# Performance work log

Hardware: AMD Instinct MI355X
Metric: run time of the kernel (lower is better)

The kernel has to match this reference:

```python
import jax, jax.numpy as jnp
import numpy as np

D_MODEL = 2048
N_HEADS = 16
KV_HEADS = 4
HEAD_DIM = D_MODEL // N_HEADS  # 128
B, T = 2, 2048


def setup_inputs() -> dict:
    key = jax.random.key(0)
    ks = jax.random.split(key, 8)
    s = 1.0 / np.sqrt(D_MODEL)
    x = jax.random.normal(ks[0], (B, T, D_MODEL), dtype=jnp.float32)
    # Linear weights stored as (in_features, out_features); y = x @ W
    Wq = jax.random.normal(ks[1], (D_MODEL, D_MODEL), dtype=jnp.float32) * s
    Wk = jax.random.normal(ks[2], (D_MODEL, KV_HEADS * HEAD_DIM), dtype=jnp.float32) * s
    Wv = jax.random.normal(ks[3], (D_MODEL, KV_HEADS * HEAD_DIM), dtype=jnp.float32) * s
    Wo = jax.random.normal(ks[4], (D_MODEL, D_MODEL), dtype=jnp.float32) * s
    weight_logits = jnp.ones((KV_HEADS,), dtype=jnp.float32)
    weight_values = jnp.ones((KV_HEADS,), dtype=jnp.float32)
    # additive causal mask (1, 1, T, T): 0 on/below diag, -inf above
    neg_inf = jnp.float32(-1e30)
    causal = jnp.tril(jnp.ones((T, T), dtype=bool))
    attn_mask = jnp.where(causal, jnp.float32(0.0), neg_inf)[None, None]
    return {"x": x, "attn_mask": attn_mask, "Wq": Wq, "Wk": Wk, "Wv": Wv,
            "Wo": Wo, "weight_logits": weight_logits, "weight_values": weight_values}


def reference(x, attn_mask, Wq, Wk, Wv, Wo, weight_logits, weight_values):
    Bx, Tx, _ = x.shape
    H, G, D = N_HEADS, KV_HEADS, HEAD_DIM
    group_size = H // G
    head_to_group = jnp.arange(H) // group_size  # (H,)

    q = (x @ Wq).reshape(Bx, Tx, H, D).transpose(0, 2, 1, 3)  # (B,H,T,D)
    k = (x @ Wk).reshape(Bx, Tx, G, D).transpose(0, 2, 1, 3)  # (B,G,T,D)
    v = (x @ Wv).reshape(Bx, Tx, G, D).transpose(0, 2, 1, 3)  # (B,G,T,D)

    # GQA expansion: gather kv groups per head
    k_g = k[:, head_to_group]  # (B,H,T,D)
    v_g = v[:, head_to_group]  # (B,H,T,D)
    # (use_value_weight=False: weight_values unused)

    logit_scale = weight_logits[head_to_group][None, :, None, None]  # (1,H,1,1)
    inv_sqrt_d = jnp.float32(1.0 / np.sqrt(D))
    logits = jnp.einsum('bhqd,bhkd->bhqk', q, k_g) * inv_sqrt_d * logit_scale
    logits = logits + attn_mask
    attn = jax.nn.softmax(logits, axis=-1)  # dropout p=0 -> identity
    y = jnp.einsum('bhqk,bhkd->bhqd', attn, v_g)
    y = y.transpose(0, 2, 1, 3).reshape(Bx, Tx, H * D)
    return y @ Wo
```

## Files before the change

### kernel.cpp

```cpp
#include <hip/hip_runtime.h>
#include <hip/hip_bf16.h>

#define TT 2048
#define DM 2048
#define NH 16
#define KVH 4
#define HD 128

typedef __attribute__((ext_vector_type(8))) short bs8;
typedef __attribute__((ext_vector_type(4))) float fx4;
typedef __attribute__((ext_vector_type(4))) unsigned short us4;
typedef __attribute__((ext_vector_type(8))) unsigned short us8;

#if __has_builtin(__builtin_amdgcn_exp2f)
#define EXP2(x) __builtin_amdgcn_exp2f(x)
#else
#define EXP2(x) exp2f(x)
#endif

__device__ inline unsigned short f2b(float f) {
  __hip_bfloat16 h = __float2bfloat16(f);
  return *reinterpret_cast<unsigned short*>(&h);
}

__device__ inline float b2f(unsigned short u) {
  unsigned int v = ((unsigned int)u) << 16;
  return *reinterpret_cast<float*>(&v);
}

__device__ inline void gld_lds16(const ushort* g, ushort* l) {
  __builtin_amdgcn_global_load_lds(
      (const __attribute__((address_space(1))) void*)g,
      (__attribute__((address_space(3))) void*)l,
      16, 0, 0);
}

__global__ __launch_bounds__(256) void prep_kernel(
    const float* __restrict__ x, const float* __restrict__ Wq,
    const float* __restrict__ Wk, const float* __restrict__ Wv,
    const float* __restrict__ Wo, ushort* __restrict__ xb,
    ushort* __restrict__ Wqkvt, ushort* __restrict__ Wot) {
  int tx = threadIdx.x, ty = threadIdx.y;
  if (blockIdx.z == 2) {
    int lin = (blockIdx.y * 96 + blockIdx.x) * 256 + ty * 32 + tx;
#pragma unroll
    for (int it = 0; it < 2; ++it) {
      int i = lin + it * (6144 * 256);
      if (i < (TT * 2 * DM) / 4) {
        float4 v = ((const float4*)x)[i];
        us4 o = {f2b(v.x), f2b(v.y), f2b(v.z), f2b(v.w)};
        ((us4*)xb)[i] = o;
      }
    }
    return;
  }
  __shared__ float t[32][33];
  int n0 = blockIdx.x * 32, k0 = blockIdx.y * 32;
  if (blockIdx.z == 0) {
    const float* src;
    int srcN, col0;
    if (n0 < 2048) { src = Wq; srcN = 2048; col0 = n0; }
    else if (n0 < 2560) { src = Wk; srcN = 512; col0 = n0 - 2048; }
    else { src = Wv; srcN = 512; col0 = n0 - 2560; }
    for (int jj = 0; jj < 4; ++jj)
      t[ty + jj * 8][tx] = src[(size_t)(k0 + ty + jj * 8) * srcN + col0 + tx];
    __syncthreads();
    for (int jj = 0; jj < 4; ++jj)
      Wqkvt[(size_t)(n0 + ty + jj * 8) * 2048 + k0 + tx] = f2b(t[tx][ty + jj * 8]);
  } else {
    if (n0 >= 2048) return;
    for (int jj = 0; jj < 4; ++jj)
      t[ty + jj * 8][tx] = Wo[(size_t)(k0 + ty + jj * 8) * 2048 + n0 + tx];
    __syncthreads();
    for (int jj = 0; jj < 4; ++jj)
      Wot[(size_t)(n0 + ty + jj * 8) * 2048 + k0 + tx] = f2b(t[tx][ty + jj * 8]);
  }
}

#define EPI_STRIDE 136
__global__ __launch_bounds__(256) void gemm_qkv(const ushort* __restrict__ A,
                                                const ushort* __restrict__ Bt,
                                                ushort* __restrict__ qo,
                                                ushort* __restrict__ ko,
                                                ushort* __restrict__ vo,
                                                int K) {
  __shared__ alignas(16) ushort smem[128 * EPI_STRIDE];
  ushort* As = smem;
  ushort* Bs = smem + 8192;
  const int tid = threadIdx.x;
  const int lane = tid & 63;
  const int wid = tid >> 6;
  const int wm = wid >> 1, wn = wid & 1;
  const int quad = lane >> 4, l16 = lane & 15;
  const int bm = blockIdx.y * 128, bn = blockIdx.x * 128;

  fx4 acc[4][4];
  for (int i = 0; i < 4; ++i)
    for (int j = 0; j < 4; ++j) acc[i][j] = (fx4){0.f, 0.f, 0.f, 0.f};

  const int r8 = lane >> 3, s8 = lane & 7;
  for (int k0 = 0; k0 < K; k0 += 64) {
    for (int i = 0; i < 4; ++i) {
      int m = i * 32 + wid * 8 + r8;
      int c = s8 ^ (m & 7);
      gld_lds16(A + (size_t)(bm + m) * K + k0 + c * 8, As + (i * 32 + wid * 8) * 64);
      gld_lds16(Bt + (size_t)(bn + m) * K + k0 + c * 8, Bs + (i * 32 + wid * 8) * 64);
    }
    __syncthreads();
    for (int ks = 0; ks < 2; ++ks) {
      bs8 af[4], bf[4];
      for (int mt = 0; mt < 4; ++mt) {
        int m = wm * 64 + mt * 16 + l16;
        int c = ks * 4 + quad;
        int slot = c ^ (m & 7);
        af[mt] = *(const bs8*)(As + m * 64 + slot * 8);
      }
      for (int nt = 0; nt < 4; ++nt) {
        int n = wn * 64 + nt * 16 + l16;
        int c = ks * 4 + quad;
        int slot = c ^ (n & 7);
        bf[nt] = *(const bs8*)(Bs + n * 64 + slot * 8);
      }
      for (int mt = 0; mt < 4; ++mt)
        for (int nt = 0; nt < 4; ++nt)
          acc[mt][nt] = __builtin_amdgcn_mfma_f32_16x16x32_bf16(af[mt], bf[nt],
                                                                acc[mt][nt], 0, 0, 0);
    }
    __syncthreads();
  }

  for (int mt = 0; mt < 4; ++mt)
    for (int nt = 0; nt < 4; ++nt)
      for (int r = 0; r < 4; ++r) {
        int row = wm * 64 + mt * 16 + quad * 4 + r;
        int col = wn * 64 + nt * 16 + l16;
        smem[row * EPI_STRIDE + col] = f2b(acc[mt][nt][r]);
      }
  __syncthreads();
  if (bn < 2560) {
    const int rsel = tid >> 4;
    const int csel = tid & 15;
    for (int ii = 0; ii < 8; ++ii) {
      int row = ii * 16 + rsel;
      us8 chunk = *(const us8*)(smem + row * EPI_STRIDE + csel * 8);
      int row_g = bm + row;
      int colc = bn + csel * 8;
      if (bn < 2048) {
        *(us8*)(qo + (size_t)row_g * 2048 + colc) = chunk;
      } else {
        int b = row_g >> 11, t = row_g & 2047;
        int kc = colc - 2048;
        int gg = kc >> 7, d = kc & 127;
        *(us8*)(ko + ((size_t)(b * KVH + gg) * TT + t) * HD + d) = chunk;
      }
    }
  } else {
    const int gg = (bn - 2560) >> 7;
    const int b = bm >> 11;
    const int t0 = bm & 2047;
    const int tc = tid & 15;
    const int drow = tid >> 4;
    for (int it = 0; it < 8; ++it) {
      int d = it * 16 + drow;
      us8 pw;
#pragma unroll
      for (int j = 0; j < 8; ++j) {
        int jj = (j + tc) & 7;
        pw[jj] = smem[(tc * 8 + jj) * EPI_STRIDE + d];
      }
      *(us8*)(vo + ((size_t)(b * KVH + gg) * HD + d) * TT + t0 + tc * 8) = pw;
    }
  }
}

__global__ __launch_bounds__(256) void gemm_out(const ushort* __restrict__ A,
                                                const ushort* __restrict__ Bt,
                                                float* __restrict__ Cout,
                                                int N, int K) {
  __shared__ alignas(16) ushort smem[128 * EPI_STRIDE];
  ushort* As = smem;
  ushort* Bs = smem + 8192;
  const int tid = threadIdx.x;
  const int lane = tid & 63;
  const int wid = tid >> 6;
  const int wm = wid >> 1, wn = wid & 1;
  const int quad = lane >> 4, l16 = lane & 15;
  const int bm = blockIdx.y * 128, bn = blockIdx.x * 128;

  fx4 acc[4][4];
  for (int i = 0; i < 4; ++i)
    for (int j = 0; j < 4; ++j) acc[i][j] = (fx4){0.f, 0.f, 0.f, 0.f};

  const int r8 = lane >> 3, s8 = lane & 7;
  for (int k0 = 0; k0 < K; k0 += 64) {
    for (int i = 0; i < 4; ++i) {
      int m = i * 32 + wid * 8 + r8;
      int c = s8 ^ (m & 7);
      gld_lds16(A + (size_t)(bm + m) * K + k0 + c * 8, As + (i * 32 + wid * 8) * 64);
      gld_lds16(Bt + (size_t)(bn + m) * K + k0 + c * 8, Bs + (i * 32 + wid * 8) * 64);
    }
    __syncthreads();
    for (int ks = 0; ks < 2; ++ks) {
      bs8 af[4], bf[4];
      for (int mt = 0; mt < 4; ++mt) {
        int m = wm * 64 + mt * 16 + l16;
        int c = ks * 4 + quad;
        int slot = c ^ (m & 7);
        af[mt] = *(const bs8*)(As + m * 64 + slot * 8);
      }
      for (int nt = 0; nt < 4; ++nt) {
        int n = wn * 64 + nt * 16 + l16;
        int c = ks * 4 + quad;
        int slot = c ^ (n & 7);
        bf[nt] = *(const bs8*)(Bs + n * 64 + slot * 8);
      }
      for (int mt = 0; mt < 4; ++mt)
        for (int nt = 0; nt < 4; ++nt)
          acc[mt][nt] = __builtin_amdgcn_mfma_f32_16x16x32_bf16(af[mt], bf[nt],
                                                                acc[mt][nt], 0, 0, 0);
    }
    __syncthreads();
  }

  for (int mt = 0; mt < 4; ++mt)
    for (int nt = 0; nt < 4; ++nt)
      for (int r = 0; r < 4; ++r) {
        int row = wm * 64 + mt * 16 + quad * 4 + r;
        int col = wn * 64 + nt * 16 + l16;
        smem[row * EPI_STRIDE + col] = f2b(acc[mt][nt][r]);
      }
  __syncthreads();
  const int rsel = tid >> 4;
  const int csel = tid & 15;
  for (int ii = 0; ii < 8; ++ii) {
    int row = ii * 16 + rsel;
    us8 chunk = *(const us8*)(smem + row * EPI_STRIDE + csel * 8);
    int row_g = bm + row;
    int colc = bn + csel * 8;
    float4 lo = {b2f(chunk[0]), b2f(chunk[1]), b2f(chunk[2]), b2f(chunk[3])};
    float4 hi = {b2f(chunk[4]), b2f(chunk[5]), b2f(chunk[6]), b2f(chunk[7])};
    *(float4*)(Cout + (size_t)row_g * N + colc) = lo;
    *(float4*)(Cout + (size_t)row_g * N + colc + 4) = hi;
  }
}

__global__ __launch_bounds__(512, 4) void attn_kernel(const ushort* __restrict__ qb,
                                                      const ushort* __restrict__ kb,
                                                      const ushort* __restrict__ vt,
                                                      ushort* __restrict__ yb,
                                                      const float* __restrict__ wlog) {
  __shared__ alignas(16) ushort Ks[2][64 * 128];
  __shared__ alignas(16) ushort Vs[2][128 * 64];
  __shared__ alignas(16) ushort Ps[128 * 64];

  const int bid = blockIdx.x;
  const int qt = (bid & 256) ? (bid & 15) : 15 - (bid & 15);
  const int h = (bid >> 4) & 15;
  const int b = bid >> 8;
  const int g = h >> 2;
  const int tid = threadIdx.x;
  const int lane = tid & 63;
  const int wid = tid >> 6;
  const int quad = lane >> 4;
  const int l16 = lane & 15;
  const int qw = qt * 128 + wid * 16;

  const float scale = wlog[g] * 0.08838834764831845f;
  const float sc2 = scale * 1.4426950408889634f;

  const ushort* kbase = kb + (size_t)(b * KVH + g) * TT * HD;
  const ushort* vbase = vt + (size_t)(b * KVH + g) * HD * TT;

  const ushort* kp;
  const ushort* vp;
  {
    int keyr = wid * 4 + (lane >> 4);
    int si = lane & 15;
    int ck = (si & 8) | ((si ^ keyr) & 7);
    kp = kbase + (size_t)keyr * HD + ck * 8;
    int dr = wid * 8 + (lane >> 3);
    int s8 = lane & 7;
    int cv = s8 ^ (dr & 7);
    vp = vbase + (size_t)dr * TT + cv * 8;
  }

  gld_lds16(kp, &Ks[0][wid * 512]);
  gld_lds16(kp + 32 * HD, &Ks[0][4096 + wid * 512]);
  gld_lds16(vp, &Vs[0][wid * 512]);
  gld_lds16(vp + 64 * TT, &Vs[0][4096 + wid * 512]);
  kp += 64 * HD;
  vp += 64;

  bs8 qf[4];
  {
    int q = qw + l16;
    const ushort* qrow = qb + ((size_t)(b * TT + q)) * DM + h * HD;
#pragma unroll
    for (int ks = 0; ks < 4; ++ks)
      qf[ks] = *(const bs8*)(qrow + ks * 32 + quad * 8);
  }

  float m_i = -INFINITY;
  float l_i = 0.f;
  fx4 o[8];
#pragma unroll
  for (int i = 0; i < 8; ++i) o[i] = (fx4){0.f, 0.f, 0.f, 0.f};

  const int jmax = 2 * qt + 1;
  for (int j = 0; j <= jmax; ++j) {
    const int cur = j & 1;
    if (j < jmax) {
      const int nxt = cur ^ 1;
      gld_lds16(kp, &Ks[nxt][wid * 512]);
      gld_lds16(kp + 32 * HD, &Ks[nxt][4096 + wid * 512]);
      gld_lds16(vp, &Vs[nxt][wid * 512]);
      gld_lds16(vp + 64 * TT, &Vs[nxt][4096 + wid * 512]);
      kp += 64 * HD;
      vp += 64;
      asm volatile("s_waitcnt vmcnt(4)" ::: "memory");
    } else {
      asm volatile("s_waitcnt vmcnt(0)" ::: "memory");
    }
    __builtin_amdgcn_s_barrier();

    if (j * 64 <= qw + 15) {
      const ushort* Kc = Ks[cur];
      const ushort* Vc = Vs[cur];
      fx4 s[4];
#pragma unroll
      for (int mt = 0; mt < 4; ++mt) s[mt] = (fx4){0.f, 0.f, 0.f, 0.f};
      __builtin_amdgcn_s_setprio(1);
#pragma unroll
      for (int mt = 0; mt < 4; ++mt) {
        bs8 a[4];
        int key = mt * 16 + l16;
#pragma unroll
        for (int ks = 0; ks < 4; ++ks) {
          int c = ks * 4 + quad;
          int slot = (c & 8) | ((c ^ key) & 7);
          a[ks] = *(const bs8*)(Kc + key * 128 + slot * 8);
        }
#pragma unroll
        for (int ks = 0; ks < 4; ++ks)
          s[mt] = __builtin_amdgcn_mfma_f32_16x16x32_bf16(a[ks], qf[ks],
                                                          s[mt], 0, 0, 0);
      }
      __builtin_amdgcn_s_setprio(0);

      const int q = qw + l16;
      if (j * 64 + 63 > qw) {
#pragma unroll
        for (int mt = 0; mt < 4; ++mt)
#pragma unroll
          for (int r = 0; r < 4; ++r) {
            int key = j * 64 + mt * 16 + quad * 4 + r;
            if (key > q) s[mt][r] = -1e30f;
          }
      }
      float mx = s[0][0];
#pragma unroll
      for (int mt = 0; mt < 4; ++mt)
#pragma unroll
        for (int r = 0; r < 4; ++r) mx = fmaxf(mx, s[mt][r]);
      mx = fmaxf(mx, __shfl_xor(mx, 16));
      mx = fmaxf(mx, __shfl_xor(mx, 32));

      if (!__all((mx - m_i) * scale <= 8.0f)) {
        float m_new = fmaxf(m_i, mx);
        float alpha = EXP2((m_i - m_new) * sc2);
        l_i *= alpha;
#pragma unroll
        for (int dmt = 0; dmt < 8; ++dmt)
#pragma unroll
          for (int r = 0; r < 4; ++r) o[dmt][r] *= alpha;
        m_i = m_new;
      }
      float negb = -m_i * sc2;
      float sum = 0.f;
#pragma unroll
      for (int mt = 0; mt < 4; ++mt)
#pragma unroll
        for (int r = 0; r < 4; ++r) {
          float pv = EXP2(fmaf(s[mt][r], sc2, negb));
          s[mt][r] = pv;
          sum += pv;
        }
      sum += __shfl_xor(sum, 16);
      sum += __shfl_xor(sum, 32);
      l_i += sum;

      int qrow = wid * 16 + l16;
      int sw = l16 & 7;
#pragma unroll
      for (int mt = 0; mt < 4; ++mt) {
        us4 pw = {f2b(s[mt][0]), f2b(s[mt][1]), f2b(s[mt][2]), f2b(s[mt][3])};
        int chunk = mt * 2 + (quad >> 1);
        *(us4*)(Ps + qrow * 64 + ((chunk ^ sw) << 3) + ((quad & 1) << 2)) = pw;
      }

#pragma unroll
      for (int ks = 0; ks < 2; ++ks) {
        bs8 pb = *(const bs8*)(Ps + qrow * 64 + (((ks * 4 + quad) ^ sw) << 3));
        __builtin_amdgcn_s_setprio(1);
#pragma unroll
        for (int dmt = 0; dmt < 8; ++dmt) {
          int d = dmt * 16 + l16;
          int c = ks * 4 + quad;
          int slot = c ^ (d & 7);
          bs8 va = *(const bs8*)(Vc + d * 64 + slot * 8);
          o[dmt] = __builtin_amdgcn_mfma_f32_16x16x32_bf16(va, pb, o[dmt], 0, 0, 0);
        }
        __builtin_amdgcn_s_setprio(0);
      }
    }
    asm volatile("s_waitcnt lgkmcnt(0)" ::: "memory");
    __builtin_amdgcn_s_barrier();
  }

  {
    float inv = 1.0f / l_i;
    int q = qw + l16;
    ushort* yrow = yb + ((size_t)(b * TT + q)) * DM + h * HD;
#pragma unroll
    for (int dmt = 0; dmt < 8; ++dmt) {
      us4 w = {f2b(o[dmt][0] * inv), f2b(o[dmt][1] * inv),
               f2b(o[dmt][2] * inv), f2b(o[dmt][3] * inv)};
      *(us4*)(yrow + dmt * 16 + quad * 4) = w;
    }
  }
}

extern "C" void kernel_launch(void* const* d_in, const int* in_sizes, int n_in,
                              void* d_out, int out_size, void* d_ws, size_t ws_size,
                              hipStream_t stream) {
  const float* x = (const float*)d_in[0];
  const float* Wq = (const float*)d_in[2];
  const float* Wk = (const float*)d_in[3];
  const float* Wv = (const float*)d_in[4];
  const float* Wo = (const float*)d_in[5];
  const float* wlog = (const float*)d_in[6];

  char* ws = (char*)d_ws;
  ushort* xb = (ushort*)ws;     ws += (size_t)4096 * 2048 * 2;
  ushort* Wqkvt = (ushort*)ws;  ws += (size_t)3072 * 2048 * 2;
  ushort* Wot = (ushort*)ws;    ws += (size_t)2048 * 2048 * 2;
  ushort* qbuf = (ushort*)ws;   ws += (size_t)4096 * 2048 * 2;
  ushort* kbuf = (ushort*)ws;   ws += (size_t)2 * KVH * 2048 * 128 * 2;
  ushort* vbuf = (ushort*)ws;   ws += (size_t)2 * KVH * 2048 * 128 * 2;
  ushort* ybuf = (ushort*)ws;   ws += (size_t)4096 * 2048 * 2;

  prep_kernel<<<dim3(96, 64, 3), dim3(32, 8), 0, stream>>>(
      x, Wq, Wk, Wv, Wo, xb, Wqkvt, Wot);
  gemm_qkv<<<dim3(24, 32), 256, 0, stream>>>(xb, Wqkvt, qbuf, kbuf, vbuf, 2048);
  attn_kernel<<<512, 512, 0, stream>>>(qbuf, kbuf, vbuf, ybuf, wlog);
  gemm_out<<<dim3(16, 32), 256, 0, stream>>>(ybuf, Wot, (float*)d_out, 2048, 2048);
}
```

Baseline: 318.7 us.

## Enlarge QKV GEMM tile to 256x256 with double-buffered LDS prefetch

The QKV projection GEMM moves from 128x128 tiles with 256 threads to 256x256 tiles with 512 threads and 8 waves. The next K-slice is loaded into LDS by direct global-to-LDS loads while MFMAs run on the current buffer, and MFMA issue is wrapped in s_setprio. The epilogue writes out in two column halves through LDS, and the V transpose now goes through a padded transposed LDS layout so stores are contiguous 16-byte chunks. The intent is more data reuse per block and overlap of global loads with compute. The cost is a grid of only 192 blocks, fewer than the number of CUs, plus a 128KB LDS footprint that limits occupancy.

```diff
diff --git a/kernel.cpp b/kernel.cpp
--- a/kernel.cpp
+++ b/kernel.cpp
@@ -78,97 +78,149 @@
 }
 
 #define EPI_STRIDE 136
-__global__ __launch_bounds__(256) void gemm_qkv(const ushort* __restrict__ A,
-                                                const ushort* __restrict__ Bt,
-                                                ushort* __restrict__ qo,
-                                                ushort* __restrict__ ko,
-                                                ushort* __restrict__ vo,
-                                                int K) {
-  __shared__ alignas(16) ushort smem[128 * EPI_STRIDE];
-  ushort* As = smem;
-  ushort* Bs = smem + 8192;
+#define VT_STRIDE 264
+__global__ __launch_bounds__(512, 2) void gemm_qkv(const ushort* __restrict__ A,
+                                                   const ushort* __restrict__ Bt,
+                                                   ushort* __restrict__ qo,
+                                                   ushort* __restrict__ ko,
+                                                   ushort* __restrict__ vo,
+                                                   int K) {
+  __shared__ alignas(16) ushort smem[65536];
   const int tid = threadIdx.x;
   const int lane = tid & 63;
   const int wid = tid >> 6;
-  const int wm = wid >> 1, wn = wid & 1;
+  const int wm = wid >> 2;
+  const int wn = wid & 3;
   const int quad = lane >> 4, l16 = lane & 15;
-  const int bm = blockIdx.y * 128, bn = blockIdx.x * 128;
-
-  fx4 acc[4][4];
-  for (int i = 0; i < 4; ++i)
+  const int swl = l16 & 7;
+  const int bm = blockIdx.y * 256, bn = blockIdx.x * 256;
+  const int r8 = lane >> 3, s8 = lane & 7;
+  const int cst = s8 ^ r8;
+
+  fx4 acc[8][4];
+#pragma unroll
+  for (int i = 0; i < 8; ++i)
+#pragma unroll
     for (int j = 0; j < 4; ++j) acc[i][j] = (fx4){0.f, 0.f, 0.f, 0.f};
 
-  const int r8 = lane >> 3, s8 = lane & 7;
-  for (int k0 = 0; k0 < K; k0 += 64) {
-    for (int i = 0; i < 4; ++i) {
-      int m = i * 32 + wid * 8 + r8;
-      int c = s8 ^ (m & 7);
-      gld_lds16(A + (size_t)(bm + m) * K + k0 + c * 8, As + (i * 32 + wid * 8) * 64);
-      gld_lds16(Bt + (size_t)(bn + m) * K + k0 + c * 8, Bs + (i * 32 + wid * 8) * 64);
-    }
-    __syncthreads();
-    for (int ks = 0; ks < 2; ++ks) {
-      bs8 af[4], bf[4];
-      for (int mt = 0; mt < 4; ++mt) {
-        int m = wm * 64 + mt * 16 + l16;
-        int c = ks * 4 + quad;
-        int slot = c ^ (m & 7);
-        af[mt] = *(const bs8*)(As + m * 64 + slot * 8);
-      }
+  const ushort* apA = A + (size_t)(bm + wid * 8 + r8) * K + cst * 8;
+  const ushort* apB = Bt + (size_t)(bn + wid * 8 + r8) * K + cst * 8;
+  const int dofs = (wid * 8) * 64;
+
+#pragma unroll
+  for (int s = 0; s < 4; ++s) {
+    gld_lds16(apA + (size_t)(s * 64) * K, smem + dofs + s * 4096);
+    gld_lds16(apB + (size_t)(s * 64) * K, smem + 32768 + dofs + s * 4096);
+  }
+  asm volatile("s_waitcnt vmcnt(0)" ::: "memory");
+  __builtin_amdgcn_s_barrier();
+
+  const int NT = K >> 6;
+  for (int kt = 0; kt < NT; ++kt) {
+    const int cur = kt & 1, nxt = cur ^ 1;
+    const ushort* As = smem + cur * 16384;
+    const ushort* Bs = smem + 32768 + cur * 16384;
+    if (kt + 1 < NT) {
+      const ushort* sa = apA + (kt + 1) * 64;
+      const ushort* sb = apB + (kt + 1) * 64;
+      ushort* dA = smem + nxt * 16384 + dofs;
+      ushort* dB = smem + 32768 + nxt * 16384 + dofs;
+#pragma unroll
+      for (int s = 0; s < 4; ++s) {
+        gld_lds16(sa + (size_t)(s * 64) * K, dA + s * 4096);
+        gld_lds16(sb + (size_t)(s * 64) * K, dB + s * 4096);
+      }
+    }
+#pragma unroll
+    for (int p = 0; p < 4; ++p) {
+      const int ks = p >> 1, mh = p & 1;
+      const int so = (((ks * 4 + quad) ^ swl) << 3);
+      bs8 bf[4], af[4];
+#pragma unroll
       for (int nt = 0; nt < 4; ++nt) {
         int n = wn * 64 + nt * 16 + l16;
-        int c = ks * 4 + quad;
-        int slot = c ^ (n & 7);
-        bf[nt] = *(const bs8*)(Bs + n * 64 + slot * 8);
-      }
-      for (int mt = 0; mt < 4; ++mt)
+        bf[nt] = *(const bs8*)(Bs + n * 64 + so);
+      }
+#pragma unroll
+      for (int i = 0; i < 4; ++i) {
+        int m = wm * 128 + (mh * 4 + i) * 16 + l16;
+        af[i] = *(const bs8*)(As + m * 64 + so);
+      }
+      __builtin_amdgcn_s_setprio(1);
+#pragma unroll
+      for (int i = 0; i < 4; ++i)
+#pragma unroll
         for (int nt = 0; nt < 4; ++nt)
-          acc[mt][nt] = __builtin_amdgcn_mfma_f32_16x16x32_bf16(af[mt], bf[nt],
-                                                                acc[mt][nt], 0, 0, 0);
-    }
-    __syncthreads();
-  }
-
-  for (int mt = 0; mt < 4; ++mt)
-    for (int nt = 0; nt < 4; ++nt)
-      for (int r = 0; r < 4; ++r) {
-        int row = wm * 64 + mt * 16 + quad * 4 + r;
-        int col = wn * 64 + nt * 16 + l16;
-        smem[row * EPI_STRIDE + col] = f2b(acc[mt][nt][r]);
-      }
-  __syncthreads();
+          acc[mh * 4 + i][nt] = __builtin_amdgcn_mfma_f32_16x16x32_bf16(
+              af[i], bf[nt], acc[mh * 4 + i][nt], 0, 0, 0);
+      __builtin_amdgcn_s_setprio(0);
+    }
+    if (kt + 1 < NT) asm volatile("s_waitcnt vmcnt(0)" ::: "memory");
+    __builtin_amdgcn_s_barrier();
+  }
+
   if (bn < 2560) {
-    const int rsel = tid >> 4;
-    const int csel = tid & 15;
-    for (int ii = 0; ii < 8; ++ii) {
-      int row = ii * 16 + rsel;
-      us8 chunk = *(const us8*)(smem + row * EPI_STRIDE + csel * 8);
-      int row_g = bm + row;
-      int colc = bn + csel * 8;
-      if (bn < 2048) {
-        *(us8*)(qo + (size_t)row_g * 2048 + colc) = chunk;
-      } else {
-        int b = row_g >> 11, t = row_g & 2047;
-        int kc = colc - 2048;
-        int gg = kc >> 7, d = kc & 127;
-        *(us8*)(ko + ((size_t)(b * KVH + gg) * TT + t) * HD + d) = chunk;
-      }
+#pragma unroll
+    for (int h = 0; h < 2; ++h) {
+      if ((wn >> 1) == h) {
+#pragma unroll
+        for (int mt = 0; mt < 8; ++mt)
+#pragma unroll
+          for (int nt = 0; nt < 4; ++nt)
+#pragma unroll
+            for (int r = 0; r < 4; ++r) {
+              int row = wm * 128 + mt * 16 + quad * 4 + r;
+              int col = (wn & 1) * 64 + nt * 16 + l16;
+              smem[row * EPI_STRIDE + col] = f2b(acc[mt][nt][r]);
+            }
+      }
+      __builtin_amdgcn_s_barrier();
+      const int rsel = tid >> 4;
+      const int csel = tid & 15;
+      for (int ii = 0; ii < 8; ++ii) {
+        int row = ii * 32 + rsel;
+        us8 chunk = *(const us8*)(smem + row * EPI_STRIDE + csel * 8);
+        int row_g = bm + row;
+        int colc = bn + h * 128 + csel * 8;
+        if (bn < 2048) {
+          *(us8*)(qo + (size_t)row_g * 2048 + colc) = chunk;
+        } else {
+          int b = row_g >> 11, t = row_g & 2047;
+          int kc = colc - 2048;
+          int gg = kc >> 7, d = kc & 127;
+          *(us8*)(ko + ((size_t)(b * KVH + gg) * TT + t) * HD + d) = chunk;
+        }
+      }
+      __builtin_amdgcn_s_barrier();
     }
   } else {
-    const int gg = (bn - 2560) >> 7;
     const int b = bm >> 11;
     const int t0 = bm & 2047;
-    const int tc = tid & 15;
-    const int drow = tid >> 4;
-    for (int it = 0; it < 8; ++it) {
-      int d = it * 16 + drow;
-      us8 pw;
-#pragma unroll
-      for (int j = 0; j < 8; ++j) {
-        int jj = (j + tc) & 7;
-        pw[jj] = smem[(tc * 8 + jj) * EPI_STRIDE + d];
-      }
-      *(us8*)(vo + ((size_t)(b * KVH + gg) * HD + d) * TT + t0 + tc * 8) = pw;
+#pragma unroll
+    for (int h = 0; h < 2; ++h) {
+      if ((wn >> 1) == h) {
+#pragma unroll
+        for (int mt = 0; mt < 8; ++mt)
+#pragma unroll
+          for (int nt = 0; nt < 4; ++nt)
+#pragma unroll
+            for (int r = 0; r < 4; ++r) {
+              int row = wm * 128 + mt * 16 + quad * 4 + r;
+              int col = (wn & 1) * 64 + nt * 16 + l16;
+              smem[col * VT_STRIDE + row] = f2b(acc[mt][nt][r]);
+            }
+      }
+      __builtin_amdgcn_s_barrier();
+      const int tc = tid & 31;
+      const int dr = tid >> 5;
+      for (int it = 0; it < 8; ++it) {
+        int d_local = it * 16 + dr;
+        us8 chunk = *(const us8*)(smem + d_local * VT_STRIDE + tc * 8);
+        int vc = (bn - 2560) + h * 128 + d_local;
+        int gg = vc >> 7, dd = vc & 127;
+        *(us8*)(vo + ((size_t)(b * KVH + gg) * HD + dd) * TT + t0 + tc * 8) = chunk;
+      }
+      __builtin_amdgcn_s_barrier();
     }
   }
 }
@@ -451,7 +503,7 @@
 
   prep_kernel<<<dim3(96, 64, 3), dim3(32, 8), 0, stream>>>(
       x, Wq, Wk, Wv, Wo, xb, Wqkvt, Wot);
-  gemm_qkv<<<dim3(24, 32), 256, 0, stream>>>(xb, Wqkvt, qbuf, kbuf, vbuf, 2048);
+  gemm_qkv<<<dim3(12, 16), 512, 0, stream>>>(xb, Wqkvt, qbuf, kbuf, vbuf, 2048);
   attn_kernel<<<512, 512, 0, stream>>>(qbuf, kbuf, vbuf, ybuf, wlog);
   gemm_out<<<dim3(16, 32), 256, 0, stream>>>(ybuf, Wot, (float*)d_out, 2048, 2048);
 }
```

Measured after the change: 298.0 us. 6.5% less time.
